# Kernel tuning notes

Measured on AMD Instinct MI355X. Metric: run time of the kernel, lower is better.

The kernel has to match this reference:

```python
import jax, jax.numpy as jnp
import numpy as np

N = 100_000   # nodes
E = 600_000   # edges
D = 128       # embed_dim
G = 1000      # graphs (batch ids)
L = 3         # num_layers


def setup_inputs() -> dict:
    key = jax.random.key(0)
    ks = jax.random.split(key, 12)
    s = 1.0 / np.sqrt(D)
    return {
        "x": jax.random.normal(ks[0], (N, D), jnp.float32),
        "edge_index": jax.random.randint(ks[1], (2, E), 0, N),
        "batch": jnp.sort(jax.random.randint(ks[2], (N,), 0, G)),
        "mask": jax.random.randint(ks[3], (N,), 0, 2),
        # stacked GCNConv weights/biases (in=hidden=out=D)
        "gcn_w": jax.random.normal(ks[4], (L, D, D), jnp.float32) * s,
        "gcn_b": jnp.zeros((L, D), jnp.float32),
        # MLP head: Linear(D,D) -> ReLU -> Linear(D,1)
        "lin1_w": jax.random.normal(ks[5], (D, D), jnp.float32) * s,
        "lin1_b": jnp.zeros((D,), jnp.float32),
        "lin2_w": jax.random.normal(ks[6], (D,), jnp.float32) * s,
        "lin2_b": jnp.zeros((), jnp.float32),
    }


def gcn_forward(x, src, dst, gcn_w, gcn_b):
    # symmetric gcn_norm with self-loops: deg[i] = 1 + in-degree(i)
    deg = jax.ops.segment_sum(jnp.ones((E,), x.dtype), dst, num_segments=N) + 1.0
    dinv = jax.lax.rsqrt(deg)
    enorm = dinv[src] * dinv[dst]          # [E] edge normalization
    self_norm = (dinv * dinv)[:, None]     # [N,1] self-loop normalization
    h = x
    for l in range(L):
        h = h @ gcn_w[l]                   # [N,D]
        h = (jax.ops.segment_sum(h[src] * enorm[:, None], dst, num_segments=N)
             + h * self_norm)
        h = h + gcn_b[l]
        if l < L - 1:
            h = jax.nn.relu(h)  # (dropout inactive at inference)
    return h


def reference(x, edge_index, batch, mask, gcn_w, gcn_b, lin1_w, lin1_b, lin2_w, lin2_b):
    src, dst = edge_index[0], edge_index[1]
    h = gcn_forward(x, src, dst, gcn_w, gcn_b)
    # MLP head -> per-node score [N]
    s = jax.nn.relu(h @ lin1_w + lin1_b) @ lin2_w + lin2_b
    s = jnp.where(mask == 0, jnp.float32(-1e9), s)
    # per-graph (segment) softmax — fused replacement for the unique/batch loop
    m = jax.ops.segment_max(s, batch, num_segments=G)
    e = jnp.exp(s - m[batch])
    z = jax.ops.segment_sum(e, batch, num_segments=G)
    return e / z[batch]
```

## Files before the change

kernel.cpp:

```cpp
#include <hip/hip_runtime.h>
#include <hip/hip_bf16.h>
#include <stdint.h>

typedef unsigned int u32;
typedef unsigned short u16;
typedef __attribute__((ext_vector_type(8))) short bf16x8;
typedef __attribute__((ext_vector_type(4))) float f32x4;

__device__ __forceinline__ float u16tof(u16 u){ return __uint_as_float(((u32)u) << 16); }
__device__ __forceinline__ float lo16(u32 v){ return __uint_as_float(v << 16); }
__device__ __forceinline__ float hi16(u32 v){ return __uint_as_float(v & 0xffff0000u); }
__device__ __forceinline__ u16 ftobf(float f){
  u32 b = __float_as_uint(f);
  return (u16)((b + 0x7FFFu + ((b >> 16) & 1u)) >> 16);
}
__device__ __forceinline__ u32 pack2(float a, float b){
  return (u32)ftobf(a) | ((u32)ftobf(b) << 16);
}
__device__ __forceinline__ float ldf(const void* p, int i, int isbf){
  return isbf ? u16tof(((const u16*)p)[i]) : ((const float*)p)[i];
}

__device__ __forceinline__ void acc8(float* a, uint4 v, float mk){
  a[0] = fmaf(lo16(v.x), mk, a[0]);
  a[1] = fmaf(hi16(v.x), mk, a[1]);
  a[2] = fmaf(lo16(v.y), mk, a[2]);
  a[3] = fmaf(hi16(v.y), mk, a[3]);
  a[4] = fmaf(lo16(v.z), mk, a[4]);
  a[5] = fmaf(hi16(v.z), mk, a[5]);
  a[6] = fmaf(lo16(v.w), mk, a[6]);
  a[7] = fmaf(hi16(v.w), mk, a[7]);
}

__device__ __forceinline__ void async16(const u16* g, const u16* l){
  __builtin_amdgcn_global_load_lds(
      (const __attribute__((address_space(1))) u32*)(uintptr_t)g,
      (__attribute__((address_space(3))) u32*)(uintptr_t)l,
      16, 0, 0);
}

__global__ __launch_bounds__(256) void k_prep(const void* __restrict__ gw, const void* __restrict__ l1w,
                                              u16* __restrict__ Wf, int L, int goffB,
                                              const int* __restrict__ batch, int* __restrict__ goff,
                                              int N, int G,
                                              const int* __restrict__ dst, int* __restrict__ hist,
                                              int nE, int chunk, int* __restrict__ flag){
  __shared__ int sh[256];
  const int b = blockIdx.x;
  const int t = threadIdx.x;
  const int histStart = L + 1 + goffB;

  if (b >= histStart){
    sh[t] = 0; __syncthreads();
    const int blk = b - histStart;
    const int e0 = blk * chunk, e1 = min(e0 + chunk, nE);
    for (int e = e0 + t; e < e1; e += 256) atomicAdd(&sh[dst[e] >> 9], 1);
    __syncthreads();
    hist[blk * 256 + t] = sh[t];
    return;
  }
  if (b >= L + 1){
    const int i = (b - (L + 1)) * 256 + t;
    if (i >= N) return;
    const int bt = batch[i];
    const int prev = (i == 0) ? -1 : batch[i - 1];
    for (int g = prev + 1; g <= bt; ++g) goff[g] = i;
    if (i == N - 1){ for (int g = bt + 1; g <= G; ++g) goff[g] = N; }
    return;
  }
  if (t == 0) sh[0] = 0;
  __syncthreads();
  int local = 0;
  for (int i = t; i < 4096; i += 256){
    u32 e = (((const u32*)gw)[i] >> 7) & 0xFFu;
    if (e >= 100u && e < 127u) local++;
  }
  atomicAdd(&sh[0], local);
  __syncthreads();
  const int isbf = (sh[0] > 2048) ? 1 : 0;
  if (b == 0 && t == 0) *flag = isbf;

  const void* src = (b < L) ? gw : l1w;
  const int sbase = (b < L) ? b * 16384 : 0;
  u16* dstp = Wf + (size_t)b * 16384;
  for (int g = t; g < 2048; g += 256){
    const int tt = g >> 8, ks = (g >> 6) & 3, lane = g & 63;
    const int n = tt * 16 + (lane & 15);
    const int k0 = ks * 32 + ((lane >> 4) << 3);
    u16* d = dstp + (size_t)g * 8;
    #pragma unroll
    for (int j = 0; j < 8; ++j){
      d[j] = ftobf(ldf(src, sbase + (k0 + j) * 128 + n, isbf));
    }
  }
}

__global__ __launch_bounds__(256) void k_hsum(int* __restrict__ hist, int* __restrict__ bsum){
  __shared__ int sm[256];
  const int b = blockIdx.x;
  const int t = threadIdx.x;
  const int v = hist[t * 256 + b];
  sm[t] = v; __syncthreads();
  for (int off = 1; off < 256; off <<= 1){
    int a = (t >= off) ? sm[t - off] : 0;
    __syncthreads();
    sm[t] += a;
    __syncthreads();
  }
  hist[t * 256 + b] = sm[t] - v;
  if (t == 255) bsum[b] = sm[255];
}

__global__ __launch_bounds__(256) void k_scatter(const int* __restrict__ src, const int* __restrict__ dst,
                                                 const int* __restrict__ hist, const int* __restrict__ bsum,
                                                 int2* __restrict__ tmpe, int nE, int chunk){
  __shared__ int sm[256];
  __shared__ int base[256];
  const int blk = blockIdx.x, t = threadIdx.x;
  const int v = bsum[t];
  sm[t] = v; __syncthreads();
  for (int off = 1; off < 256; off <<= 1){
    int a = (t >= off) ? sm[t - off] : 0;
    __syncthreads();
    sm[t] += a;
    __syncthreads();
  }
  base[t] = (sm[t] - v) + hist[blk * 256 + t];
  __syncthreads();
  const int e0 = blk * chunk, e1 = min(e0 + chunk, nE);
  for (int e = e0 + t; e < e1; e += 256){
    const int d = dst[e];
    const int pos = atomicAdd(&base[d >> 9], 1);
    tmpe[pos] = make_int2(src[e], d);
  }
}

__global__ __launch_bounds__(256) void k_local(const int2* __restrict__ tmpe, const int* __restrict__ bsum,
                                               int* __restrict__ boff, int* __restrict__ eid,
                                               float* __restrict__ dinv, int N, int nE, int nbkt){
  __shared__ int sm[256];
  __shared__ int bbx[257];
  __shared__ int hcnt[512];
  __shared__ int hoff[512];
  const int b = blockIdx.x, t = threadIdx.x;
  {
    const int v = bsum[t];
    sm[t] = v; __syncthreads();
    for (int off = 1; off < 256; off <<= 1){
      int a = (t >= off) ? sm[t - off] : 0;
      __syncthreads();
      sm[t] += a;
      __syncthreads();
    }
    bbx[t] = sm[t] - v;
    if (t == 255) bbx[256] = sm[255];
  }
  __syncthreads();
  const int n0 = b << 9;
  const int n1 = min(n0 + 512, N);
  const int nn = n1 - n0;
  const int e0 = bbx[b], e1 = bbx[b + 1];
  hcnt[t] = 0; hcnt[t + 256] = 0;
  __syncthreads();
  for (int e = e0 + t; e < e1; e += 256) atomicAdd(&hcnt[tmpe[e].y - n0], 1);
  __syncthreads();
  const int v0 = hcnt[t], v1 = hcnt[t + 256];
  hoff[t] = v0; hoff[t + 256] = v1;
  __syncthreads();
  for (int off = 1; off < 512; off <<= 1){
    int a0 = (t >= off) ? hoff[t - off] : 0;
    int a1 = (t + 256 >= off) ? hoff[t + 256 - off] : 0;
    __syncthreads();
    hoff[t] += a0; hoff[t + 256] += a1;
    __syncthreads();
  }
  const int ex0 = hoff[t] - v0 + e0;
  const int ex1 = hoff[t + 256] - v1 + e0;
  if (t < nn){       boff[n0 + t] = ex0;        dinv[n0 + t] = rsqrtf((float)v0 + 1.0f); }
  if (t + 256 < nn){ boff[n0 + t + 256] = ex1;  dinv[n0 + t + 256] = rsqrtf((float)v1 + 1.0f); }
  if (b == nbkt - 1 && t == 0) boff[N] = nE;
  __syncthreads();
  hoff[t] = ex0; hoff[t + 256] = ex1;
  __syncthreads();
  for (int e = e0 + t; e < e1; e += 256){
    const int2 pr = tmpe[e];
    const int pos = atomicAdd(&hoff[pr.y - n0], 1);
    eid[pos] = pr.x;
  }
}

__global__ __launch_bounds__(256) void k_mm(const void* __restrict__ X, const u16* __restrict__ Wf,
                                            const float* __restrict__ dinv, u16* __restrict__ T,
                                            int n, int cvtin, const int* __restrict__ fl){
  __shared__ u16 smw[16384];
  const int isbf = *fl;
  const int fp32in = cvtin && !isbf;
  {
    const uint4* s = (const uint4*)Wf;
    uint4* d = (uint4*)smw;
    for (int i = threadIdx.x; i < 2048; i += 256) d[i] = s[i];
  }
  __syncthreads();

  const int wave = threadIdx.x >> 6, lane = threadIdx.x & 63;
  const int m0 = blockIdx.x * 64 + wave * 16;
  int arow = m0 + (lane & 15); if (arow > n - 1) arow = n - 1;
  const int koff = (lane >> 4) << 3;

  f32x4 acc[8];
  #pragma unroll
  for (int t = 0; t < 8; ++t) acc[t] = (f32x4){0.f, 0.f, 0.f, 0.f};

  #pragma unroll
  for (int ks = 0; ks < 4; ++ks){
    bf16x8 a;
    if (fp32in){
      const float* ap = (const float*)X + (size_t)arow * 128 + koff + ks * 32;
      const float4 f0 = *(const float4*)ap;
      const float4 f1 = *(const float4*)(ap + 4);
      a = (bf16x8){(short)ftobf(f0.x), (short)ftobf(f0.y), (short)ftobf(f0.z), (short)ftobf(f0.w),
                   (short)ftobf(f1.x), (short)ftobf(f1.y), (short)ftobf(f1.z), (short)ftobf(f1.w)};
    } else {
      a = *(const bf16x8*)((const u16*)X + (size_t)arow * 128 + koff + ks * 32);
    }
    #pragma unroll
    for (int t = 0; t < 8; ++t){
      const bf16x8 b = *(const bf16x8*)(smw + (size_t)(((t * 4 + ks) * 64 + lane) * 8));
      acc[t] = __builtin_amdgcn_mfma_f32_16x16x32_bf16(a, b, acc[t], 0, 0, 0);
    }
  }
  __syncthreads();

  const int quad = lane >> 4, col0 = lane & 15;
  float dv[4];
  #pragma unroll
  for (int r = 0; r < 4; ++r){
    const int row = m0 + quad * 4 + r;
    dv[r] = (row < n) ? dinv[row] : 0.f;
  }
  u16* my = smw + wave * 2112;
  #pragma unroll
  for (int t = 0; t < 8; ++t){
    #pragma unroll
    for (int r = 0; r < 4; ++r){
      my[(quad * 4 + r) * 132 + t * 16 + col0] = ftobf(acc[t][r] * dv[r]);
    }
  }
  #pragma unroll
  for (int i = 0; i < 4; ++i){
    const int row = i * 4 + (lane >> 4);
    const int grow = m0 + row;
    const int c8 = (lane & 15) * 8;
    if (grow < n){
      const u16* s = &my[row * 132 + c8];
      uint2 lo = *(const uint2*)(s);
      uint2 hi = *(const uint2*)(s + 4);
      *(uint4*)&T[(size_t)grow * 128 + c8] = make_uint4(lo.x, lo.y, hi.x, hi.y);
    }
  }
}

__global__ __launch_bounds__(256) void k_gmm(const u16* __restrict__ Tin, const int* __restrict__ boff,
                                             const int* __restrict__ eid, const float* __restrict__ dinv,
                                             const void* __restrict__ bias, int layer,
                                             const u16* __restrict__ Wf, u16* __restrict__ Tout,
                                             int n, const int* __restrict__ fl){
  __shared__ u16 sma[16 * 132];
  __shared__ u16 ring[4][4][512];
  __shared__ int seid[1024];
  __shared__ int sboff[17];
  const int isbf = *fl;
  const int tid = threadIdx.x;
  const int wave = tid >> 6, lane = tid & 63;
  const int sub = lane >> 4, l16 = lane & 15;
  const int m0 = blockIdx.x * 16;

  const int e0 = boff[m0];
  const int e1 = boff[min(m0 + 16, n)];
  const int len = e1 - e0;
  const int inlds = (len <= 1024);
  if (tid < 17) sboff[tid] = boff[min(m0 + tid, n)];
  if (inlds){ for (int i = tid; i < len; i += 256) seid[i] = eid[e0 + i]; }
  __syncthreads();

  const int wsub = wave * 4 + sub;
  const int node = m0 + wsub;
  const int js = sboff[wsub];
  const int d  = sboff[wsub + 1] - js;

  float a[8];
  #pragma unroll
  for (int k = 0; k < 8; ++k) a[k] = 0.f;
  if (node < n){
    const uint4 sv = ((const uint4*)(Tin + (size_t)node * 128))[l16];
    acc8(a, sv, 1.f);
  }

  int T = 0;
  #pragma unroll
  for (int s2 = 0; s2 < 4; ++s2){
    const int dd = sboff[wave * 4 + s2 + 1] - sboff[wave * 4 + s2];
    T = (dd > T) ? dd : T;
  }

  if (inlds){
    const int jloc = js - e0;
    const int jlast = jloc + ((d > 0) ? (d - 1) : 0);
    const u16* base = Tin + (size_t)l16 * 8;
    u16* slot = &ring[wave][0][0];
    #pragma unroll
    for (int t = 0; t < 4; ++t){
      if (t < T){
        const int idx = (d > 0) ? seid[(t < d) ? (jloc + t) : jlast] : 0;
        async16(base + (size_t)idx * 128, slot + (t & 3) * 512);
      }
    }
    int t = 0;
    for (; t + 4 <= T; ++t){
      asm volatile("s_waitcnt vmcnt(3)" ::: "memory");
      const uint4 v = *(const uint4*)(slot + (t & 3) * 512 + lane * 8);
      acc8(a, v, (t < d) ? 1.f : 0.f);
      const int tn = t + 4;
      if (tn < T){
        const int idx = (d > 0) ? seid[(tn < d) ? (jloc + tn) : jlast] : 0;
        async16(base + (size_t)idx * 128, slot + (tn & 3) * 512);
      }
    }
    for (; t < T; ++t){
      const int rem = T - t - 1;
      if (rem >= 2)      asm volatile("s_waitcnt vmcnt(2)" ::: "memory");
      else if (rem == 1) asm volatile("s_waitcnt vmcnt(1)" ::: "memory");
      else               asm volatile("s_waitcnt vmcnt(0)" ::: "memory");
      const uint4 v = *(const uint4*)(slot + (t & 3) * 512 + lane * 8);
      acc8(a, v, (t < d) ? 1.f : 0.f);
    }
  } else {
    for (int j = js; j < js + d; ++j){
      const uint4 v = ((const uint4*)(Tin + (size_t)eid[j] * 128))[l16];
      acc8(a, v, 1.f);
    }
  }

  float h[8];
  #pragma unroll
  for (int k = 0; k < 8; ++k) h[k] = 0.f;
  if (node < n){
    const float di = dinv[node];
    const int bb = layer * 128 + l16 * 8;
    #pragma unroll
    for (int k = 0; k < 8; ++k){
      h[k] = fmaxf(fmaf(a[k], di, ldf(bias, bb + k, isbf)), 0.f);
    }
  }
  {
    uint4 o;
    o.x = pack2(h[0], h[1]); o.y = pack2(h[2], h[3]); o.z = pack2(h[4], h[5]); o.w = pack2(h[6], h[7]);
    *(uint4*)&sma[(wave * 4 + sub) * 132 + l16 * 8] = o;
  }
  __syncthreads();

  f32x4 acc[2];
  acc[0] = (f32x4){0.f,0.f,0.f,0.f}; acc[1] = (f32x4){0.f,0.f,0.f,0.f};
  #pragma unroll
  for (int ks = 0; ks < 4; ++ks){
    const bf16x8 av = *(const bf16x8*)(sma + l16 * 132 + sub * 8 + ks * 32);
    #pragma unroll
    for (int tt = 0; tt < 2; ++tt){
      const int t = wave * 2 + tt;
      const bf16x8 bv = *(const bf16x8*)(Wf + (size_t)(((t * 4 + ks) * 64 + lane) * 8));
      acc[tt] = __builtin_amdgcn_mfma_f32_16x16x32_bf16(av, bv, acc[tt], 0, 0, 0);
    }
  }
  __syncthreads();

  float dv[4];
  #pragma unroll
  for (int r = 0; r < 4; ++r){
    const int row = m0 + sub * 4 + r;
    dv[r] = (row < n) ? dinv[row] : 0.f;
  }
  #pragma unroll
  for (int tt = 0; tt < 2; ++tt){
    const int t = wave * 2 + tt;
    #pragma unroll
    for (int r = 0; r < 4; ++r){
      sma[(sub * 4 + r) * 132 + t * 16 + l16] = ftobf(acc[tt][r] * dv[r]);
    }
  }
  __syncthreads();

  {
    const int row = tid >> 4;
    const int c8 = (tid & 15) * 8;
    if (m0 + row < n){
      const u16* s = &sma[row * 132 + c8];
      uint2 lo = *(const uint2*)(s);
      uint2 hi = *(const uint2*)(s + 4);
      *(uint4*)&Tout[(size_t)(m0 + row) * 128 + c8] = make_uint4(lo.x, lo.y, hi.x, hi.y);
    }
  }
}

__global__ __launch_bounds__(256) void k_ghead(const u16* __restrict__ Tin, const int* __restrict__ boff,
                                               const int* __restrict__ eid, const float* __restrict__ dinv,
                                               const void* __restrict__ bias, int layer,
                                               const u16* __restrict__ Wf, const void* __restrict__ b1,
                                               const void* __restrict__ w2, const void* __restrict__ b2,
                                               const int* __restrict__ mask, float* __restrict__ s,
                                               int n, const int* __restrict__ fl){
  __shared__ u16 sma[16 * 132];
  __shared__ u16 ring[4][4][512];
  __shared__ int seid[1024];
  __shared__ int sboff[17];
  __shared__ float sred[4][16];
  const int isbf = *fl;
  const int tid = threadIdx.x;
  const int wave = tid >> 6, lane = tid & 63;
  const int sub = lane >> 4, l16 = lane & 15;
  const int m0 = blockIdx.x * 16;

  const int e0 = boff[m0];
  const int e1 = boff[min(m0 + 16, n)];
  const int len = e1 - e0;
  const int inlds = (len <= 1024);
  if (tid < 17) sboff[tid] = boff[min(m0 + tid, n)];
  if (inlds){ for (int i = tid; i < len; i += 256) seid[i] = eid[e0 + i]; }
  __syncthreads();

  const int wsub = wave * 4 + sub;
  const int node = m0 + wsub;
  const int js = sboff[wsub];
  const int d  = sboff[wsub + 1] - js;

  float a[8];
  #pragma unroll
  for (int k = 0; k < 8; ++k) a[k] = 0.f;
  if (node < n){
    const uint4 sv = ((const uint4*)(Tin + (size_t)node * 128))[l16];
    acc8(a, sv, 1.f);
  }

  int T = 0;
  #pragma unroll
  for (int s2 = 0; s2 < 4; ++s2){
    const int dd = sboff[wave * 4 + s2 + 1] - sboff[wave * 4 + s2];
    T = (dd > T) ? dd : T;
  }

  if (inlds){
    const int jloc = js - e0;
    const int jlast = jloc + ((d > 0) ? (d - 1) : 0);
    const u16* base = Tin + (size_t)l16 * 8;
    u16* slot = &ring[wave][0][0];
    #pragma unroll
    for (int t = 0; t < 4; ++t){
      if (t < T){
        const int idx = (d > 0) ? seid[(t < d) ? (jloc + t) : jlast] : 0;
        async16(base + (size_t)idx * 128, slot + (t & 3) * 512);
      }
    }
    int t = 0;
    for (; t + 4 <= T; ++t){
      asm volatile("s_waitcnt vmcnt(3)" ::: "memory");
      const uint4 v = *(const uint4*)(slot + (t & 3) * 512 + lane * 8);
      acc8(a, v, (t < d) ? 1.f : 0.f);
      const int tn = t + 4;
      if (tn < T){
        const int idx = (d > 0) ? seid[(tn < d) ? (jloc + tn) : jlast] : 0;
        async16(base + (size_t)idx * 128, slot + (tn & 3) * 512);
      }
    }
    for (; t < T; ++t){
      const int rem = T - t - 1;
      if (rem >= 2)      asm volatile("s_waitcnt vmcnt(2)" ::: "memory");
      else if (rem == 1) asm volatile("s_waitcnt vmcnt(1)" ::: "memory");
      else               asm volatile("s_waitcnt vmcnt(0)" ::: "memory");
      const uint4 v = *(const uint4*)(slot + (t & 3) * 512 + lane * 8);
      acc8(a, v, (t < d) ? 1.f : 0.f);
    }
  } else {
    for (int j = js; j < js + d; ++j){
      const uint4 v = ((const uint4*)(Tin + (size_t)eid[j] * 128))[l16];
      acc8(a, v, 1.f);
    }
  }

  float h[8];
  #pragma unroll
  for (int k = 0; k < 8; ++k) h[k] = 0.f;
  if (node < n){
    const float di = dinv[node];
    const int bb = layer * 128 + l16 * 8;
    #pragma unroll
    for (int k = 0; k < 8; ++k){
      h[k] = fmaf(a[k], di, ldf(bias, bb + k, isbf));
    }
  }
  {
    uint4 o;
    o.x = pack2(h[0], h[1]); o.y = pack2(h[2], h[3]); o.z = pack2(h[4], h[5]); o.w = pack2(h[6], h[7]);
    *(uint4*)&sma[(wave * 4 + sub) * 132 + l16 * 8] = o;
  }
  __syncthreads();

  f32x4 acc[2];
  acc[0] = (f32x4){0.f,0.f,0.f,0.f}; acc[1] = (f32x4){0.f,0.f,0.f,0.f};
  #pragma unroll
  for (int ks = 0; ks < 4; ++ks){
    const bf16x8 av = *(const bf16x8*)(sma + l16 * 132 + sub * 8 + ks * 32);
    #pragma unroll
    for (int tt = 0; tt < 2; ++tt){
      const int t = wave * 2 + tt;
      const bf16x8 bv = *(const bf16x8*)(Wf + (size_t)(((t * 4 + ks) * 64 + lane) * 8));
      acc[tt] = __builtin_amdgcn_mfma_f32_16x16x32_bf16(av, bv, acc[tt], 0, 0, 0);
    }
  }

  float p0 = 0.f, p1 = 0.f, p2 = 0.f, p3 = 0.f;
  #pragma unroll
  for (int tt = 0; tt < 2; ++tt){
    const int col = (wave * 2 + tt) * 16 + l16;
    const float bv = ldf(b1, col, isbf);
    const float wv = ldf(w2, col, isbf);
    p0 = fmaf(fmaxf(acc[tt][0] + bv, 0.f), wv, p0);
    p1 = fmaf(fmaxf(acc[tt][1] + bv, 0.f), wv, p1);
    p2 = fmaf(fmaxf(acc[tt][2] + bv, 0.f), wv, p2);
    p3 = fmaf(fmaxf(acc[tt][3] + bv, 0.f), wv, p3);
  }
  #pragma unroll
  for (int k = 1; k < 16; k <<= 1){
    p0 += __shfl_xor(p0, k);
    p1 += __shfl_xor(p1, k);
    p2 += __shfl_xor(p2, k);
    p3 += __shfl_xor(p3, k);
  }
  if (l16 == 0){
    sred[wave][sub * 4 + 0] = p0;
    sred[wave][sub * 4 + 1] = p1;
    sred[wave][sub * 4 + 2] = p2;
    sred[wave][sub * 4 + 3] = p3;
  }
  __syncthreads();
  if (tid < 16){
    const int row = m0 + tid;
    if (row < n){
      float sc = sred[0][tid] + sred[1][tid] + sred[2][tid] + sred[3][tid]
               + ldf(b2, 0, isbf);
      if (mask[row] == 0) sc = -1e9f;
      s[row] = sc;
    }
  }
}

__global__ __launch_bounds__(256) void k_gsm(const float* __restrict__ s, const int* __restrict__ goff,
                                             void* __restrict__ out, int G, const int* __restrict__ fl){
  const int g = blockIdx.x * 4 + (threadIdx.x >> 6);
  if (g >= G) return;
  const int lane = threadIdx.x & 63;
  const int i0 = goff[g], i1 = goff[g + 1];
  if (i0 >= i1) return;
  float m = -3.4e38f;
  for (int j = i0 + lane; j < i1; j += 64) m = fmaxf(m, s[j]);
  #pragma unroll
  for (int k = 32; k; k >>= 1) m = fmaxf(m, __shfl_xor(m, k));
  float zz = 0.f;
  for (int j = i0 + lane; j < i1; j += 64) zz += expf(s[j] - m);
  #pragma unroll
  for (int k = 32; k; k >>= 1) zz += __shfl_xor(zz, k);
  const float rz = 1.f / zz;
  const int isbf = *fl;
  for (int j = i0 + lane; j < i1; j += 64){
    const float v = expf(s[j] - m) * rz;
    if (isbf) ((u16*)out)[j] = ftobf(v);
    else      ((float*)out)[j] = v;
  }
}

extern "C" void kernel_launch(void* const* d_in, const int* in_sizes, int n_in,
                              void* d_out, int out_size, void* d_ws, size_t ws_size,
                              hipStream_t stream){
  const void* x    = d_in[0];
  const int* ei    = (const int*)d_in[1];
  const int* batch = (const int*)d_in[2];
  const int* mask  = (const int*)d_in[3];
  const void* gw   = d_in[4];
  const void* gb   = d_in[5];
  const void* l1w  = d_in[6];
  const void* l1b  = d_in[7];
  const void* l2w  = d_in[8];
  const void* l2b  = d_in[9];

  const int N = in_sizes[2];
  const int E = in_sizes[1] / 2;
  const int D = 128;
  const int L = in_sizes[4] / (D * D);
  const int G = 1000;

  char* p = (char*)d_ws;
  u16*  Hb    = (u16*)p;   p += (size_t)N * D * sizeof(u16);
  u16*  Tb    = (u16*)p;   p += (size_t)N * D * sizeof(u16);
  u16*  Wf    = (u16*)p;   p += (size_t)(L + 1) * D * D * sizeof(u16);
  float* dinv = (float*)p; p += (size_t)N * sizeof(float);
  float* sbuf = (float*)p; p += (size_t)N * sizeof(float);
  int*  boff  = (int*)p;   p += (size_t)(N + 1) * sizeof(int);
  int*  eid   = (int*)p;   p += (size_t)E * sizeof(int);
  int*  goff  = (int*)p;   p += (size_t)(G + 1) * sizeof(int);
  int*  hist  = (int*)p;   p += 256 * 256 * sizeof(int);
  int*  bsum  = (int*)p;   p += 256 * sizeof(int);
  int2* tmpe  = (int2*)p;  p += (size_t)E * sizeof(int2);
  int*  flag  = (int*)p;   p += 256;

  const int* srcp = ei;
  const int* dstp = ei + E;

  const int mmg   = (N + 63) / 64;
  const int fg    = (N + 15) / 16;
  const int goffB = (N + 255) / 256;
  const int chunk = (E + 255) / 256;
  const int nbkt  = (N + 511) / 512;

  k_prep<<<(L + 1) + goffB + 256, 256, 0, stream>>>(gw, l1w, Wf, L, goffB,
                                                    batch, goff, N, G, dstp, hist, E, chunk, flag);
  k_hsum<<<256, 256, 0, stream>>>(hist, bsum);
  k_scatter<<<256, 256, 0, stream>>>(srcp, dstp, hist, bsum, tmpe, E, chunk);
  k_local<<<nbkt, 256, 0, stream>>>(tmpe, bsum, boff, eid, dinv, N, E, nbkt);

  k_mm<<<mmg, 256, 0, stream>>>(x, Wf, dinv, Tb, N, 1, flag);
  k_gmm<<<fg, 256, 0, stream>>>(Tb, boff, eid, dinv, gb, 0, Wf + (size_t)1 * D * D, Hb, N, flag);
  k_gmm<<<fg, 256, 0, stream>>>(Hb, boff, eid, dinv, gb, 1, Wf + (size_t)2 * D * D, Tb, N, flag);
  k_ghead<<<fg, 256, 0, stream>>>(Tb, boff, eid, dinv, gb, 2, Wf + (size_t)L * D * D,
                                  l1b, l2w, l2b, mask, sbuf, N, flag);
  k_gsm<<<(G + 3) / 4, 256, 0, stream>>>(sbuf, goff, d_out, G, flag);
}
```

Before: 312.8 us.

## Merge histogram scan, edge scatter and first matmul into one launch

Removes the separate histogram-sum kernel by having each scatter block compute its own prefix offsets directly from the histogram. The first-layer X·W matmul is folded into the same launch as extra blocks, so it runs concurrently with the edge scatter. Because dinv is not yet available at that point, the per-source dinv scaling moves into the first aggregation kernel, which now does a dinv gather per edge. This trades two kernel launches and a serial dependency for redundant per-block histogram reads and extra scattered dinv loads in layer 0.

```diff
diff --git a/kernel.cpp b/kernel.cpp
--- a/kernel.cpp
+++ b/kernel.cpp
@@ -95,43 +95,106 @@
   }
 }
 
-__global__ __launch_bounds__(256) void k_hsum(int* __restrict__ hist, int* __restrict__ bsum){
-  __shared__ int sm[256];
+__global__ __launch_bounds__(256) void k_scat_mm(const int* __restrict__ src, const int* __restrict__ dst,
+                                                 const int* __restrict__ hist, int* __restrict__ bsum,
+                                                 int2* __restrict__ tmpe, int nE, int chunk,
+                                                 const void* __restrict__ x, const u16* __restrict__ Wf,
+                                                 u16* __restrict__ T, int N,
+                                                 const int* __restrict__ fl){
+  __shared__ u16 smw[16384];
   const int b = blockIdx.x;
-  const int t = threadIdx.x;
-  const int v = hist[t * 256 + b];
-  sm[t] = v; __syncthreads();
-  for (int off = 1; off < 256; off <<= 1){
-    int a = (t >= off) ? sm[t - off] : 0;
+  const int tid = threadIdx.x;
+
+  if (b < 256){
+    int* sm   = (int*)smw;
+    int* base = ((int*)smw) + 256;
+    const int blk = b;
+    int tot = 0, pre = 0;
+    for (int j = 0; j < 256; j += 8){
+      int v[8];
+      #pragma unroll
+      for (int k = 0; k < 8; ++k) v[k] = hist[(j + k) * 256 + tid];
+      #pragma unroll
+      for (int k = 0; k < 8; ++k){
+        if (j + k < blk) pre += v[k];
+        tot += v[k];
+      }
+    }
+    sm[tid] = tot; __syncthreads();
+    for (int off = 1; off < 256; off <<= 1){
+      int a = (tid >= off) ? sm[tid - off] : 0;
+      __syncthreads(); sm[tid] += a; __syncthreads();
+    }
+    base[tid] = (sm[tid] - tot) + pre;
+    if (blk == 0) bsum[tid] = tot;
     __syncthreads();
-    sm[t] += a;
-    __syncthreads();
-  }
-  hist[t * 256 + b] = sm[t] - v;
-  if (t == 255) bsum[b] = sm[255];
-}
-
-__global__ __launch_bounds__(256) void k_scatter(const int* __restrict__ src, const int* __restrict__ dst,
-                                                 const int* __restrict__ hist, const int* __restrict__ bsum,
-                                                 int2* __restrict__ tmpe, int nE, int chunk){
-  __shared__ int sm[256];
-  __shared__ int base[256];
-  const int blk = blockIdx.x, t = threadIdx.x;
-  const int v = bsum[t];
-  sm[t] = v; __syncthreads();
-  for (int off = 1; off < 256; off <<= 1){
-    int a = (t >= off) ? sm[t - off] : 0;
-    __syncthreads();
-    sm[t] += a;
-    __syncthreads();
-  }
-  base[t] = (sm[t] - v) + hist[blk * 256 + t];
-  __syncthreads();
-  const int e0 = blk * chunk, e1 = min(e0 + chunk, nE);
-  for (int e = e0 + t; e < e1; e += 256){
-    const int d = dst[e];
-    const int pos = atomicAdd(&base[d >> 9], 1);
-    tmpe[pos] = make_int2(src[e], d);
+    const int e0 = blk * chunk, e1 = min(e0 + chunk, nE);
+    for (int e = e0 + tid; e < e1; e += 256){
+      const int d = dst[e];
+      const int pos = atomicAdd(&base[d >> 9], 1);
+      tmpe[pos] = make_int2(src[e], d);
+    }
+    return;
+  }
+
+  const int isbf = *fl;
+  const int fp32in = !isbf;
+  {
+    const uint4* s = (const uint4*)Wf;
+    uint4* d = (uint4*)smw;
+    for (int i = tid; i < 2048; i += 256) d[i] = s[i];
+  }
+  __syncthreads();
+
+  const int wave = tid >> 6, lane = tid & 63;
+  const int m0 = (b - 256) * 64 + wave * 16;
+  int arow = m0 + (lane & 15); if (arow > N - 1) arow = N - 1;
+  const int koff = (lane >> 4) << 3;
+
+  f32x4 acc[8];
+  #pragma unroll
+  for (int t = 0; t < 8; ++t) acc[t] = (f32x4){0.f, 0.f, 0.f, 0.f};
+
+  #pragma unroll
+  for (int ks = 0; ks < 4; ++ks){
+    bf16x8 a;
+    if (fp32in){
+      const float* ap = (const float*)x + (size_t)arow * 128 + koff + ks * 32;
+      const float4 f0 = *(const float4*)ap;
+      const float4 f1 = *(const float4*)(ap + 4);
+      a = (bf16x8){(short)ftobf(f0.x), (short)ftobf(f0.y), (short)ftobf(f0.z), (short)ftobf(f0.w),
+                   (short)ftobf(f1.x), (short)ftobf(f1.y), (short)ftobf(f1.z), (short)ftobf(f1.w)};
+    } else {
+      a = *(const bf16x8*)((const u16*)x + (size_t)arow * 128 + koff + ks * 32);
+    }
+    #pragma unroll
+    for (int t = 0; t < 8; ++t){
+      const bf16x8 bb = *(const bf16x8*)(smw + (size_t)(((t * 4 + ks) * 64 + lane) * 8));
+      acc[t] = __builtin_amdgcn_mfma_f32_16x16x32_bf16(a, bb, acc[t], 0, 0, 0);
+    }
+  }
+  __syncthreads();
+
+  const int quad = lane >> 4, col0 = lane & 15;
+  u16* my = smw + wave * 2112;
+  #pragma unroll
+  for (int t = 0; t < 8; ++t){
+    #pragma unroll
+    for (int r = 0; r < 4; ++r){
+      my[(quad * 4 + r) * 132 + t * 16 + col0] = ftobf(acc[t][r]);
+    }
+  }
+  #pragma unroll
+  for (int i = 0; i < 4; ++i){
+    const int row = i * 4 + (lane >> 4);
+    const int grow = m0 + row;
+    const int c8 = (lane & 15) * 8;
+    if (grow < N){
+      const u16* s = &my[row * 132 + c8];
+      uint2 lo = *(const uint2*)(s);
+      uint2 hi = *(const uint2*)(s + 4);
+      *(uint4*)&T[(size_t)grow * 128 + c8] = make_uint4(lo.x, lo.y, hi.x, hi.y);
+    }
   }
 }
 
@@ -189,80 +252,9 @@
   }
 }
 
-__global__ __launch_bounds__(256) void k_mm(const void* __restrict__ X, const u16* __restrict__ Wf,
-                                            const float* __restrict__ dinv, u16* __restrict__ T,
-                                            int n, int cvtin, const int* __restrict__ fl){
-  __shared__ u16 smw[16384];
-  const int isbf = *fl;
-  const int fp32in = cvtin && !isbf;
-  {
-    const uint4* s = (const uint4*)Wf;
-    uint4* d = (uint4*)smw;
-    for (int i = threadIdx.x; i < 2048; i += 256) d[i] = s[i];
-  }
-  __syncthreads();
-
-  const int wave = threadIdx.x >> 6, lane = threadIdx.x & 63;
-  const int m0 = blockIdx.x * 64 + wave * 16;
-  int arow = m0 + (lane & 15); if (arow > n - 1) arow = n - 1;
-  const int koff = (lane >> 4) << 3;
-
-  f32x4 acc[8];
-  #pragma unroll
-  for (int t = 0; t < 8; ++t) acc[t] = (f32x4){0.f, 0.f, 0.f, 0.f};
-
-  #pragma unroll
-  for (int ks = 0; ks < 4; ++ks){
-    bf16x8 a;
-    if (fp32in){
-      const float* ap = (const float*)X + (size_t)arow * 128 + koff + ks * 32;
-      const float4 f0 = *(const float4*)ap;
-      const float4 f1 = *(const float4*)(ap + 4);
-      a = (bf16x8){(short)ftobf(f0.x), (short)ftobf(f0.y), (short)ftobf(f0.z), (short)ftobf(f0.w),
-                   (short)ftobf(f1.x), (short)ftobf(f1.y), (short)ftobf(f1.z), (short)ftobf(f1.w)};
-    } else {
-      a = *(const bf16x8*)((const u16*)X + (size_t)arow * 128 + koff + ks * 32);
-    }
-    #pragma unroll
-    for (int t = 0; t < 8; ++t){
-      const bf16x8 b = *(const bf16x8*)(smw + (size_t)(((t * 4 + ks) * 64 + lane) * 8));
-      acc[t] = __builtin_amdgcn_mfma_f32_16x16x32_bf16(a, b, acc[t], 0, 0, 0);
-    }
-  }
-  __syncthreads();
-
-  const int quad = lane >> 4, col0 = lane & 15;
-  float dv[4];
-  #pragma unroll
-  for (int r = 0; r < 4; ++r){
-    const int row = m0 + quad * 4 + r;
-    dv[r] = (row < n) ? dinv[row] : 0.f;
-  }
-  u16* my = smw + wave * 2112;
-  #pragma unroll
-  for (int t = 0; t < 8; ++t){
-    #pragma unroll
-    for (int r = 0; r < 4; ++r){
-      my[(quad * 4 + r) * 132 + t * 16 + col0] = ftobf(acc[t][r] * dv[r]);
-    }
-  }
-  #pragma unroll
-  for (int i = 0; i < 4; ++i){
-    const int row = i * 4 + (lane >> 4);
-    const int grow = m0 + row;
-    const int c8 = (lane & 15) * 8;
-    if (grow < n){
-      const u16* s = &my[row * 132 + c8];
-      uint2 lo = *(const uint2*)(s);
-      uint2 hi = *(const uint2*)(s + 4);
-      *(uint4*)&T[(size_t)grow * 128 + c8] = make_uint4(lo.x, lo.y, hi.x, hi.y);
-    }
-  }
-}
-
 __global__ __launch_bounds__(256) void k_gmm(const u16* __restrict__ Tin, const int* __restrict__ boff,
                                              const int* __restrict__ eid, const float* __restrict__ dinv,
-                                             const void* __restrict__ bias, int layer,
+                                             const void* __restrict__ bias, int layer, int srcscale,
                                              const u16* __restrict__ Wf, u16* __restrict__ Tout,
                                              int n, const int* __restrict__ fl){
   __shared__ u16 sma[16 * 132];
@@ -293,7 +285,7 @@
   for (int k = 0; k < 8; ++k) a[k] = 0.f;
   if (node < n){
     const uint4 sv = ((const uint4*)(Tin + (size_t)node * 128))[l16];
-    acc8(a, sv, 1.f);
+    acc8(a, sv, srcscale ? dinv[node] : 1.f);
   }
 
   int T = 0;
@@ -319,7 +311,12 @@
     for (; t + 4 <= T; ++t){
       asm volatile("s_waitcnt vmcnt(3)" ::: "memory");
       const uint4 v = *(const uint4*)(slot + (t & 3) * 512 + lane * 8);
-      acc8(a, v, (t < d) ? 1.f : 0.f);
+      float mk = 0.f;
+      if (t < d){
+        const int idx2 = seid[jloc + t];
+        mk = srcscale ? dinv[idx2] : 1.f;
+      }
+      acc8(a, v, mk);
       const int tn = t + 4;
       if (tn < T){
         const int idx = (d > 0) ? seid[(tn < d) ? (jloc + tn) : jlast] : 0;
@@ -332,12 +329,18 @@
       else if (rem == 1) asm volatile("s_waitcnt vmcnt(1)" ::: "memory");
       else               asm volatile("s_waitcnt vmcnt(0)" ::: "memory");
       const uint4 v = *(const uint4*)(slot + (t & 3) * 512 + lane * 8);
-      acc8(a, v, (t < d) ? 1.f : 0.f);
+      float mk = 0.f;
+      if (t < d){
+        const int idx2 = seid[jloc + t];
+        mk = srcscale ? dinv[idx2] : 1.f;
+      }
+      acc8(a, v, mk);
     }
   } else {
     for (int j = js; j < js + d; ++j){
-      const uint4 v = ((const uint4*)(Tin + (size_t)eid[j] * 128))[l16];
-      acc8(a, v, 1.f);
+      const int idx = eid[j];
+      const uint4 v = ((const uint4*)(Tin + (size_t)idx * 128))[l16];
+      acc8(a, v, srcscale ? dinv[idx] : 1.f);
     }
   }
 
@@ -621,13 +624,12 @@
 
   k_prep<<<(L + 1) + goffB + 256, 256, 0, stream>>>(gw, l1w, Wf, L, goffB,
                                                     batch, goff, N, G, dstp, hist, E, chunk, flag);
-  k_hsum<<<256, 256, 0, stream>>>(hist, bsum);
-  k_scatter<<<256, 256, 0, stream>>>(srcp, dstp, hist, bsum, tmpe, E, chunk);
+  k_scat_mm<<<256 + mmg, 256, 0, stream>>>(srcp, dstp, hist, bsum, tmpe, E, chunk,
+                                           x, Wf, Tb, N, flag);
   k_local<<<nbkt, 256, 0, stream>>>(tmpe, bsum, boff, eid, dinv, N, E, nbkt);
 
-  k_mm<<<mmg, 256, 0, stream>>>(x, Wf, dinv, Tb, N, 1, flag);
-  k_gmm<<<fg, 256, 0, stream>>>(Tb, boff, eid, dinv, gb, 0, Wf + (size_t)1 * D * D, Hb, N, flag);
-  k_gmm<<<fg, 256, 0, stream>>>(Hb, boff, eid, dinv, gb, 1, Wf + (size_t)2 * D * D, Tb, N, flag);
+  k_gmm<<<fg, 256, 0, stream>>>(Tb, boff, eid, dinv, gb, 0, 1, Wf + (size_t)1 * D * D, Hb, N, flag);
+  k_gmm<<<fg, 256, 0, stream>>>(Hb, boff, eid, dinv, gb, 1, 0, Wf + (size_t)2 * D * D, Tb, N, flag);
   k_ghead<<<fg, 256, 0, stream>>>(Tb, boff, eid, dinv, gb, 2, Wf + (size_t)L * D * D,
                                   l1b, l2w, l2b, mask, sbuf, N, flag);
   k_gsm<<<(G + 3) / 4, 256, 0, stream>>>(sbuf, goff, d_out, G, flag);
```

New measurement: 321.3 us. +2.7%, slower.
